# Performance work log

Measured on AMD Instinct MI355X. Metric: run time of the kernel, lower is better.

The kernel has to match this reference:

```python
import jax, jax.numpy as jnp
import numpy as np
from jax import lax

D_MODEL, D_INNER, D_STATE, D_CONV, DT_RANK = 1024, 2048, 16, 4, 64
B, L = 1, 2048


def setup_inputs() -> dict:
    key = jax.random.key(0)
    ks = jax.random.split(key, 10)
    s = lambda d: 1.0 / np.sqrt(d)
    return {
        "x": jax.random.normal(ks[0], (B, L, D_MODEL), jnp.float32),
        "W_in": jax.random.normal(ks[1], (D_MODEL, 2 * D_INNER), jnp.float32) * s(D_MODEL),
        "conv_w": jax.random.normal(ks[2], (D_INNER, D_CONV), jnp.float32) * s(D_CONV),
        "conv_b": jax.random.normal(ks[3], (D_INNER,), jnp.float32) * 0.01,
        "W_x": jax.random.normal(ks[4], (D_INNER, DT_RANK + 2 * D_STATE), jnp.float32) * s(D_INNER),
        "W_dt": jax.random.normal(ks[5], (DT_RANK, D_INNER), jnp.float32) * s(DT_RANK),
        "b_dt": jax.random.normal(ks[6], (D_INNER,), jnp.float32) * 0.01,
        # A = arange(1, d_state+1) repeated over d_inner; A_log = log(A)
        "A_log": jnp.log(jnp.tile(jnp.arange(1.0, D_STATE + 1.0, dtype=jnp.float32), (D_INNER, 1))),
        "D": jnp.ones((D_INNER,), jnp.float32),
        "W_out": jax.random.normal(ks[7], (D_INNER, D_MODEL), jnp.float32) * s(D_INNER),
    }


def reference(x, W_in, conv_w, conv_b, W_x, W_dt, b_dt, A_log, D, W_out):
    b, l, dm = x.shape
    di, n = A_log.shape[0], A_log.shape[1]
    # input projection + split into conv branch and gate residual
    x_and_res = x @ W_in                          # (b, l, 2*di)
    xc, res = x_and_res[..., :di], x_and_res[..., di:]
    # causal depthwise conv1d (left pad k-1, matches torch padding=k-1 + slice[:l])
    k = conv_w.shape[1]
    xp = jnp.pad(xc, ((0, 0), (k - 1, 0), (0, 0)))
    xconv = conv_b
    for j in range(k):
        xconv = xconv + xp[:, j:j + l, :] * conv_w[:, j]
    xs = jax.nn.silu(xconv)                       # (b, l, di)
    # selection parameters
    x_dbl = xs @ W_x                              # (b, l, dt_rank + 2n)
    dt_r = x_dbl[..., :DT_RANK]
    Bm = x_dbl[..., DT_RANK:DT_RANK + n]          # (b, l, n)
    Cm = x_dbl[..., DT_RANK + n:]                 # (b, l, n)
    dt = jax.nn.softplus(dt_r @ W_dt + b_dt)      # (b, l, di)
    A = -jnp.exp(A_log)                           # (di, n)
    # discretize
    dA = jnp.exp(jnp.einsum('bld,dn->bldn', dt, A))
    dBx = jnp.einsum('bld,bln->bldn', dt, Bm) * xs[..., None]
    # sequential state scan over time
    def step(h, inp):
        dA_t, dBx_t, C_t = inp                    # (b,di,n),(b,di,n),(b,n)
        h = dA_t * h + dBx_t
        y = jnp.einsum('bdn,bn->bd', h, C_t)
        return h, y
    h0 = jnp.zeros((b, di, n), x.dtype)
    hT, ys = lax.scan(step, h0, (dA.transpose(1, 0, 2, 3),
                                 dBx.transpose(1, 0, 2, 3),
                                 Cm.transpose(1, 0, 2)))
    y = ys.transpose(1, 0, 2) + xs * D            # (b, l, di)
    y = y * jax.nn.silu(res)
    out = y @ W_out                               # (b, l, d_model)
    return out, hT
```

## Files before the change

### kernel.cpp

```cpp
#include <hip/hip_runtime.h>
#include <math.h>

#define DM 1024
#define DI 2048
#define NS 16
#define DTR 64
#define LL 2048
#define NXDBL 96
#define NCHUNK 64
#define CHLEN 32
#define KSPLIT 8
#define G2KC 256

typedef unsigned short u16;
typedef __attribute__((ext_vector_type(8))) short short8;
typedef __attribute__((ext_vector_type(4))) float f32x4;

__device__ __forceinline__ float sigmoidf_(float x) { return 1.f / (1.f + __expf(-x)); }
__device__ __forceinline__ float siluf_(float x) { return x * sigmoidf_(x); }
__device__ __forceinline__ float softplus_fast(float x) {
    return fmaxf(x, 0.f) + __logf(1.f + __expf(-fabsf(x)));
}
__device__ __forceinline__ u16 f2b(float f) {
    unsigned u = __float_as_uint(f);
    return (u16)((u + 0x7FFFu + ((u >> 16) & 1u)) >> 16);
}

__global__ __launch_bounds__(256) void convert_plain(const float* __restrict__ src,
                                                     u16* __restrict__ dst) {
    const int i = (blockIdx.x * 256 + threadIdx.x) * 4;
    float4 v = *(const float4*)&src[i];
    u16 o[4] = {f2b(v.x), f2b(v.y), f2b(v.z), f2b(v.w)};
    *(ushort4*)&dst[i] = *(ushort4*)o;
}

__global__ __launch_bounds__(256) void convert_T(const float* __restrict__ src,
                                                 u16* __restrict__ dst, int R, int C) {
    __shared__ float t[32][33];
    const int tx = threadIdx.x & 31, ty = threadIdx.x >> 5;
    const int c0 = blockIdx.x * 32, r0 = blockIdx.y * 32;
#pragma unroll
    for (int i = 0; i < 4; i++)
        t[ty + i * 8][tx] = src[(size_t)(r0 + ty + i * 8) * C + c0 + tx];
    __syncthreads();
#pragma unroll
    for (int i = 0; i < 4; i++)
        dst[(size_t)(c0 + ty + i * 8) * R + r0 + tx] = f2b(t[tx][ty + i * 8]);
}

#define WAITV(N) asm volatile("s_waitcnt vmcnt(" #N ")" ::: "memory")
template <int EPI, int NSTEPS>
__global__ __launch_bounds__(256) void gemm_mfma(const u16* __restrict__ A,
                                                 const u16* __restrict__ Bt,
                                                 float* __restrict__ C0,
                                                 float* __restrict__ C1,
                                                 int M, int N, int lda) {
    __shared__ u16 As[3][128 * 32];
    __shared__ u16 Bs[3][128 * 32];
    const int tid = threadIdx.x;
    const int lane = tid & 63;
    const int wave = tid >> 6;
    const int bm = blockIdx.y * 128, bn = blockIdx.x * 128;
    const int wr = wave >> 1, wc = wave & 1;
    const int k_off = blockIdx.z * (NSTEPS * 32);

    f32x4 acc[4][4];
#pragma unroll
    for (int m = 0; m < 4; m++)
#pragma unroll
        for (int n = 0; n < 4; n++) acc[m][n] = (f32x4)0.f;

    const int srow = tid >> 2, skel = (tid & 3) << 3;
    const u16* Ag0 = A + (size_t)(bm + srow) * lda + k_off + skel;
    const u16* Ag1 = A + (size_t)(bm + 64 + srow) * lda + k_off + skel;
    const u16* Bg0 = Bt + (size_t)(bn + srow) * lda + k_off + skel;
    const u16* Bg1 = Bt + (size_t)(bn + 64 + srow) * lda + k_off + skel;
    u16* Asl = &As[0][0] + tid * 8;
    u16* Bsl = &Bs[0][0] + tid * 8;

    const int arow = (wr * 64 + (lane & 15)) * 32 + (lane >> 4) * 8;
    const int brow = (wc * 64 + (lane & 15)) * 32 + (lane >> 4) * 8;

#define STAGE(buf, ks)                                                               \
    do {                                                                             \
        __builtin_amdgcn_global_load_lds(                                            \
            (const __attribute__((address_space(1))) unsigned*)(Ag0 + (ks)),         \
            (__attribute__((address_space(3))) unsigned*)(Asl + (buf) * 4096),       \
            16, 0, 0);                                                               \
        __builtin_amdgcn_global_load_lds(                                            \
            (const __attribute__((address_space(1))) unsigned*)(Ag1 + (ks)),         \
            (__attribute__((address_space(3))) unsigned*)(Asl + (buf) * 4096 + 2048),\
            16, 0, 0);                                                               \
        __builtin_amdgcn_global_load_lds(                                            \
            (const __attribute__((address_space(1))) unsigned*)(Bg0 + (ks)),         \
            (__attribute__((address_space(3))) unsigned*)(Bsl + (buf) * 4096),       \
            16, 0, 0);                                                               \
        __builtin_amdgcn_global_load_lds(                                            \
            (const __attribute__((address_space(1))) unsigned*)(Bg1 + (ks)),         \
            (__attribute__((address_space(3))) unsigned*)(Bsl + (buf) * 4096 + 2048),\
            16, 0, 0);                                                               \
    } while (0)

#define COMPUTE(buf)                                                                 \
    do {                                                                             \
        short8 av[4], bv[4];                                                         \
        _Pragma("unroll") for (int m = 0; m < 4; m++)                                \
            av[m] = *(const short8*)&As[buf][arow + m * 512];                        \
        _Pragma("unroll") for (int n = 0; n < 4; n++)                                \
            bv[n] = *(const short8*)&Bs[buf][brow + n * 512];                        \
        _Pragma("unroll") for (int m = 0; m < 4; m++)                                \
            _Pragma("unroll") for (int n = 0; n < 4; n++)                            \
                acc[m][n] = __builtin_amdgcn_mfma_f32_16x16x32_bf16(av[m], bv[n],    \
                                                                    acc[m][n], 0, 0, 0); \
    } while (0)

    STAGE(0, 0);
    if (NSTEPS > 1) STAGE(1, 32);
#pragma unroll
    for (int s = 0; s < NSTEPS; ++s) {
        if (s + 2 < NSTEPS) {
            STAGE((s + 2) % 3, (s + 2) * 32);
            WAITV(8);
        } else if (s + 1 < NSTEPS) {
            WAITV(4);
        } else {
            WAITV(0);
        }
        __builtin_amdgcn_s_barrier();
        COMPUTE(s % 3);
        __builtin_amdgcn_s_barrier();
    }
#undef STAGE
#undef COMPUTE

    const int crow0 = bm + wr * 64 + (lane >> 4) * 4;
    const int ccol0 = bn + wc * 64 + (lane & 15);
    float* C0z = C0 + (size_t)blockIdx.z * M * N;
#pragma unroll
    for (int m = 0; m < 4; m++)
#pragma unroll
        for (int n = 0; n < 4; n++) {
            const int col = ccol0 + n * 16;
#pragma unroll
            for (int r = 0; r < 4; r++) {
                const int row = crow0 + m * 16 + r;
                const float v = acc[m][n][r];
                if (EPI == 1) {
                    if (col < DI)
                        C0[(size_t)row * DI + col] = v;
                    else
                        C1[(size_t)row * DI + col - DI] = v;
                } else {
                    C0z[(size_t)row * N + col] = v;
                }
            }
        }
}

__global__ __launch_bounds__(256) void gemm128_dt(const float* __restrict__ A,
                                                  const float* __restrict__ B,
                                                  const float* __restrict__ bias,
                                                  float* __restrict__ C,
                                                  int N, int K, int lda) {
    __shared__ float As[16][128];
    __shared__ float Bs[16][128];
    const int tid = threadIdx.x;
    const int bm = blockIdx.y * 128, bn = blockIdx.x * 128;
    const int ty = tid >> 4, tx = tid & 15;
    float acc[8][8];
#pragma unroll
    for (int i = 0; i < 8; i++)
#pragma unroll
        for (int j = 0; j < 8; j++) acc[i][j] = 0.f;

    const int ar = tid >> 2, ak = (tid & 3) << 2;
    const int bk = tid >> 5, bc = (tid & 31) << 2;

    for (int k0 = 0; k0 < K; k0 += 16) {
        float4 a0 = *(const float4*)&A[(size_t)(bm + ar) * lda + k0 + ak];
        float4 a1 = *(const float4*)&A[(size_t)(bm + ar + 64) * lda + k0 + ak];
        float4 b0 = *(const float4*)&B[(size_t)(k0 + bk) * N + bn + bc];
        float4 b1 = *(const float4*)&B[(size_t)(k0 + bk + 8) * N + bn + bc];
        __syncthreads();
        As[ak + 0][ar] = a0.x; As[ak + 1][ar] = a0.y;
        As[ak + 2][ar] = a0.z; As[ak + 3][ar] = a0.w;
        As[ak + 0][ar + 64] = a1.x; As[ak + 1][ar + 64] = a1.y;
        As[ak + 2][ar + 64] = a1.z; As[ak + 3][ar + 64] = a1.w;
        *(float4*)&Bs[bk][bc] = b0;
        *(float4*)&Bs[bk + 8][bc] = b1;
        __syncthreads();
#pragma unroll
        for (int k = 0; k < 16; k++) {
            float a[8], b[8];
            *(float4*)&a[0] = *(const float4*)&As[k][ty * 8];
            *(float4*)&a[4] = *(const float4*)&As[k][ty * 8 + 4];
            *(float4*)&b[0] = *(const float4*)&Bs[k][tx * 8];
            *(float4*)&b[4] = *(const float4*)&Bs[k][tx * 8 + 4];
#pragma unroll
            for (int i = 0; i < 8; i++)
#pragma unroll
                for (int j = 0; j < 8; j++) acc[i][j] = fmaf(a[i], b[j], acc[i][j]);
        }
    }
#pragma unroll
    for (int i = 0; i < 8; i++) {
        const int row = bm + ty * 8 + i;
#pragma unroll
        for (int j = 0; j < 8; j += 4) {
            const int col = bn + tx * 8 + j;
            const float4 bi = *(const float4*)&bias[col];
            float4 v = make_float4(softplus_fast(acc[i][j] + bi.x),
                                   softplus_fast(acc[i][j + 1] + bi.y),
                                   softplus_fast(acc[i][j + 2] + bi.z),
                                   softplus_fast(acc[i][j + 3] + bi.w));
            *(float4*)&C[(size_t)row * N + col] = v;
        }
    }
}

__global__ __launch_bounds__(256) void sum2(const float* __restrict__ p,
                                            float* __restrict__ out, int n) {
    const int i = (blockIdx.x * 256 + threadIdx.x) * 4;
    float4 a = *(const float4*)&p[i];
    float4 b = *(const float4*)&p[(size_t)n + i];
    float4 o = make_float4(a.x + b.x, a.y + b.y, a.z + b.z, a.w + b.w);
    *(float4*)&out[i] = o;
}

__global__ __launch_bounds__(256) void conv_silu(const float* __restrict__ xc,
                                                 const float* __restrict__ cw,
                                                 const float* __restrict__ cb,
                                                 float* __restrict__ xs) {
    const int gid = blockIdx.x * 256 + threadIdx.x;
    const int l = gid >> 11;
    const int d = gid & (DI - 1);
    const float4 w = *(const float4*)&cw[d * 4];
    float acc = cb[d];
    const float wj[4] = {w.x, w.y, w.z, w.w};
#pragma unroll
    for (int j = 0; j < 4; j++) {
        const int li = l + j - 3;
        if (li >= 0) acc = fmaf(xc[(size_t)li * DI + d], wj[j], acc);
    }
    xs[gid] = siluf_(acc);
}

__global__ __launch_bounds__(256) void gemm2_splitk(const float* __restrict__ xs,
                                                    const float* __restrict__ Wx,
                                                    float* __restrict__ part) {
    __shared__ float As[32][64];
    __shared__ float Bs[32 * 96];
    const int tid = threadIdx.x;
    const int bm = blockIdx.x * 64;
    const int ks = blockIdx.y;
    const int ty = tid >> 4, tx = tid & 15;
    float acc[4][6];
#pragma unroll
    for (int i = 0; i < 4; i++)
#pragma unroll
        for (int j = 0; j < 6; j++) acc[i][j] = 0.f;

    for (int kt = 0; kt < G2KC; kt += 32) {
        const int kbase = ks * G2KC + kt;
        float4 av[2];
        int arr[2], akk[2];
#pragma unroll
        for (int i = 0; i < 2; i++) {
            const int f = tid + 256 * i;
            arr[i] = f >> 3;
            akk[i] = (f & 7) << 2;
            av[i] = *(const float4*)&xs[(size_t)(bm + arr[i]) * DI + kbase + akk[i]];
        }
        float4 bv[3];
        int bro[3], bco[3];
#pragma unroll
        for (int i = 0; i < 3; i++) {
            const int f = tid + 256 * i;
            bro[i] = (f << 2) / 96;
            bco[i] = (f << 2) % 96;
            bv[i] = *(const float4*)&Wx[(size_t)(kbase + bro[i]) * 96 + bco[i]];
        }
        __syncthreads();
#pragma unroll
        for (int i = 0; i < 2; i++) {
            As[akk[i] + 0][arr[i]] = av[i].x;
            As[akk[i] + 1][arr[i]] = av[i].y;
            As[akk[i] + 2][arr[i]] = av[i].z;
            As[akk[i] + 3][arr[i]] = av[i].w;
        }
#pragma unroll
        for (int i = 0; i < 3; i++)
            *(float4*)&Bs[bro[i] * 96 + bco[i]] = bv[i];
        __syncthreads();
#pragma unroll
        for (int k = 0; k < 32; k++) {
            float a[4], b[6];
            *(float4*)&a[0] = *(const float4*)&As[k][ty * 4];
            *(float2*)&b[0] = *(const float2*)&Bs[k * 96 + tx * 6];
            *(float2*)&b[2] = *(const float2*)&Bs[k * 96 + tx * 6 + 2];
            *(float2*)&b[4] = *(const float2*)&Bs[k * 96 + tx * 6 + 4];
#pragma unroll
            for (int i = 0; i < 4; i++)
#pragma unroll
                for (int j = 0; j < 6; j++) acc[i][j] = fmaf(a[i], b[j], acc[i][j]);
        }
    }
#pragma unroll
    for (int i = 0; i < 4; i++) {
        const int row = bm + ty * 4 + i;
#pragma unroll
        for (int j = 0; j < 6; j++) {
            part[((size_t)ks * LL + row) * NXDBL + tx * 6 + j] = acc[i][j];
        }
    }
}

__global__ __launch_bounds__(256) void gemm2_reduce(const float* __restrict__ part,
                                                    float* __restrict__ xdbl) {
    const int gid = blockIdx.x * 256 + threadIdx.x;
    if (gid < LL * NXDBL) {
        float s = 0.f;
#pragma unroll
        for (int ks = 0; ks < KSPLIT; ks++) s += part[(size_t)ks * LL * NXDBL + gid];
        xdbl[gid] = s;
    }
}

__global__ __launch_bounds__(256) void scan_phase1(const float* __restrict__ dt,
                                                   const float* __restrict__ xs,
                                                   const float* __restrict__ xdbl,
                                                   const float* __restrict__ A_log,
                                                   float* __restrict__ chA,
                                                   float* __restrict__ chB) {
    const int g = blockIdx.x * 256 + threadIdx.x;
    const int d = g & (DI - 1);
    const int c = g >> 11;
    float An2[NS], ap[NS], bc[NS];
    {
        float al[NS];
#pragma unroll
        for (int q = 0; q < 4; q++)
            *(float4*)&al[q * 4] = *(const float4*)&A_log[d * NS + q * 4];
#pragma unroll
        for (int n = 0; n < NS; n++) {
            An2[n] = -__expf(al[n]) * 1.44269504f;
            ap[n] = 1.f;
            bc[n] = 0.f;
        }
    }
    const int l0 = c * CHLEN;
    for (int l = l0; l < l0 + CHLEN; ++l) {
        const float dtv = dt[(size_t)l * DI + d];
        const float xsv = xs[(size_t)l * DI + d];
        const float dx = dtv * xsv;
        float bv[NS];
#pragma unroll
        for (int q = 0; q < 4; q++)
            *(float4*)&bv[q * 4] = *(const float4*)&xdbl[(size_t)l * NXDBL + DTR + q * 4];
#pragma unroll
        for (int n = 0; n < NS; n++) {
            const float al = __builtin_amdgcn_exp2f(dtv * An2[n]);
            ap[n] *= al;
            bc[n] = fmaf(al, bc[n], dx * bv[n]);
        }
    }
    const size_t o = ((size_t)c * DI + d) * NS;
#pragma unroll
    for (int q = 0; q < 4; q++) {
        *(float4*)&chA[o + q * 4] = *(float4*)&ap[q * 4];
        *(float4*)&chB[o + q * 4] = *(float4*)&bc[q * 4];
    }
}

__global__ __launch_bounds__(256) void scan_phase2(float* __restrict__ chA,
                                                   const float* __restrict__ chB,
                                                   float* __restrict__ hT_out) {
    const int t = blockIdx.x * 256 + threadIdx.x;
    float h = 0.f;
#pragma unroll 4
    for (int c = 0; c < NCHUNK; ++c) {
        const size_t o = (size_t)c * DI * NS + t;
        const float a = chA[o];
        const float b = chB[o];
        chA[o] = h;
        h = fmaf(a, h, b);
    }
    hT_out[t] = h;
}

__global__ __launch_bounds__(256) void scan_phase3(const float* __restrict__ dt,
                                                   const float* __restrict__ xs,
                                                   const float* __restrict__ xdbl,
                                                   const float* __restrict__ A_log,
                                                   const float* __restrict__ h0,
                                                   const float* __restrict__ Dw,
                                                   const float* __restrict__ res,
                                                   u16* __restrict__ yb) {
    const int g = blockIdx.x * 256 + threadIdx.x;
    const int d = g & (DI - 1);
    const int c = g >> 11;
    float An2[NS], h[NS];
    {
        float al[NS];
#pragma unroll
        for (int q = 0; q < 4; q++)
            *(float4*)&al[q * 4] = *(const float4*)&A_log[d * NS + q * 4];
#pragma unroll
        for (int n = 0; n < NS; n++) An2[n] = -__expf(al[n]) * 1.44269504f;
    }
    const size_t ho = ((size_t)c * DI + d) * NS;
#pragma unroll
    for (int q = 0; q < 4; q++) *(float4*)&h[q * 4] = *(const float4*)&h0[ho + q * 4];
    const float Dd = Dw[d];
    const int l0 = c * CHLEN;
    for (int l = l0; l < l0 + CHLEN; ++l) {
        const float dtv = dt[(size_t)l * DI + d];
        const float xsv = xs[(size_t)l * DI + d];
        const float resv = res[(size_t)l * DI + d];
        const float dx = dtv * xsv;
        float bv[NS], cv[NS];
#pragma unroll
        for (int q = 0; q < 4; q++) {
            *(float4*)&bv[q * 4] = *(const float4*)&xdbl[(size_t)l * NXDBL + DTR + q * 4];
            *(float4*)&cv[q * 4] =
                *(const float4*)&xdbl[(size_t)l * NXDBL + DTR + NS + q * 4];
        }
#pragma unroll
        for (int n = 0; n < NS; n++) {
            const float al = __builtin_amdgcn_exp2f(dtv * An2[n]);
            h[n] = fmaf(al, h[n], dx * bv[n]);
        }
        float y0 = 0.f, y1 = 0.f, y2 = 0.f, y3 = 0.f;
#pragma unroll
        for (int n = 0; n < NS; n += 4) {
            y0 = fmaf(h[n + 0], cv[n + 0], y0);
            y1 = fmaf(h[n + 1], cv[n + 1], y1);
            y2 = fmaf(h[n + 2], cv[n + 2], y2);
            y3 = fmaf(h[n + 3], cv[n + 3], y3);
        }
        float yv = ((y0 + y1) + (y2 + y3)) + xsv * Dd;
        yv *= siluf_(resv);
        yb[(size_t)l * DI + d] = f2b(yv);
    }
}

extern "C" void kernel_launch(void* const* d_in, const int* in_sizes, int n_in,
                              void* d_out, int out_size, void* d_ws, size_t ws_size,
                              hipStream_t stream) {
    const float* x = (const float*)d_in[0];
    const float* W_in = (const float*)d_in[1];
    const float* conv_w = (const float*)d_in[2];
    const float* conv_b = (const float*)d_in[3];
    const float* W_x = (const float*)d_in[4];
    const float* W_dt = (const float*)d_in[5];
    const float* b_dt = (const float*)d_in[6];
    const float* A_log = (const float*)d_in[7];
    const float* Dw = (const float*)d_in[8];
    const float* W_out = (const float*)d_in[9];
    float* out = (float*)d_out;

    float* ws = (float*)d_ws;
    float* xc = ws;
    float* res = ws + 4194304;
    float* xs = ws + 8388608;
    float* dt = ws + 12582912;
    float* xdbl = ws + 16777216;
    float* chA = ws + 16973824;
    float* chB = ws + 19070976;
    u16* xb = (u16*)chB;
    float* part = chB;
    u16* W_outT_b = (u16*)chB;
    u16* W_inT_b = (u16*)dt;
    u16* yb = (u16*)xc;
    float* g4part = res;

    convert_plain<<<(LL * DM) / 1024, 256, 0, stream>>>(x, xb);
    convert_T<<<dim3(2 * DI / 32, DM / 32), 256, 0, stream>>>(W_in, W_inT_b, DM, 2 * DI);
    gemm_mfma<1, DM / 32><<<dim3(2 * DI / 128, LL / 128), 256, 0, stream>>>(
        xb, W_inT_b, xc, res, LL, 2 * DI, DM);
    conv_silu<<<(LL * DI) / 256, 256, 0, stream>>>(xc, conv_w, conv_b, xs);
    gemm2_splitk<<<dim3(LL / 64, KSPLIT), 256, 0, stream>>>(xs, W_x, part);
    gemm2_reduce<<<(LL * NXDBL + 255) / 256, 256, 0, stream>>>(part, xdbl);
    gemm128_dt<<<dim3(DI / 128, LL / 128), 256, 0, stream>>>(xdbl, W_dt, b_dt, dt,
                                                             DI, DTR, NXDBL);
    scan_phase1<<<(DI * NCHUNK) / 256, 256, 0, stream>>>(dt, xs, xdbl, A_log, chA, chB);
    scan_phase2<<<(DI * NS) / 256, 256, 0, stream>>>(chA, chB, out + (size_t)LL * DM);
    convert_T<<<dim3(DM / 32, DI / 32), 256, 0, stream>>>(W_out, W_outT_b, DI, DM);
    scan_phase3<<<(DI * NCHUNK) / 256, 256, 0, stream>>>(dt, xs, xdbl, A_log, chA, Dw,
                                                         res, yb);
    gemm_mfma<0, DI / 64><<<dim3(DM / 128, LL / 128, 2), 256, 0, stream>>>(
        yb, W_outT_b, g4part, nullptr, LL, DM, DI);
    sum2<<<(LL * DM) / 1024, 256, 0, stream>>>(g4part, out, LL * DM);
}
```

Before: 201.7 us.

## Move x_dbl projection to bf16 MFMA split-K GEMM and swizzle LDS layout

Replaces the fp32 FMA split-K GEMM for xs@W_x with the existing bf16 MFMA GEMM kernel. To feed it, conv_silu now also emits a bf16 copy of xs, W_x is transposed and zero-padded to 128 columns, and a 16-way split-K runs with a matching reduce. It also XOR-swizzles the LDS layout in the MFMA GEMM to reduce bank conflicts on fragment reads, which affects all three GEMMs. Workspace buffers are given distinct regions instead of aliasing. In exchange it adds extra launches and lowers the precision of the selection parameters to bf16.

```diff
diff --git a/kernel.cpp b/kernel.cpp
--- a/kernel.cpp
+++ b/kernel.cpp
@@ -9,8 +9,6 @@
 #define NXDBL 96
 #define NCHUNK 64
 #define CHLEN 32
-#define KSPLIT 8
-#define G2KC 256
 
 typedef unsigned short u16;
 typedef __attribute__((ext_vector_type(8))) short short8;
@@ -46,6 +44,11 @@
 #pragma unroll
     for (int i = 0; i < 4; i++)
         dst[(size_t)(c0 + ty + i * 8) * R + r0 + tx] = f2b(t[tx][ty + i * 8]);
+}
+
+__global__ __launch_bounds__(256) void fill_zero_u16(u16* __restrict__ p, int n) {
+    const int i = blockIdx.x * 256 + threadIdx.x;
+    if (i < n) p[i] = 0;
 }
 
 #define WAITV(N) asm volatile("s_waitcnt vmcnt(" #N ")" ::: "memory")
@@ -70,7 +73,9 @@
 #pragma unroll
         for (int n = 0; n < 4; n++) acc[m][n] = (f32x4)0.f;
 
-    const int srow = tid >> 2, skel = (tid & 3) << 3;
+    const int srow = tid >> 2;
+    const int swz = (tid >> 3) & 3;
+    const int skel = (((tid & 3) ^ swz) << 3);
     const u16* Ag0 = A + (size_t)(bm + srow) * lda + k_off + skel;
     const u16* Ag1 = A + (size_t)(bm + 64 + srow) * lda + k_off + skel;
     const u16* Bg0 = Bt + (size_t)(bn + srow) * lda + k_off + skel;
@@ -78,8 +83,9 @@
     u16* Asl = &As[0][0] + tid * 8;
     u16* Bsl = &Bs[0][0] + tid * 8;
 
-    const int arow = (wr * 64 + (lane & 15)) * 32 + (lane >> 4) * 8;
-    const int brow = (wc * 64 + (lane & 15)) * 32 + (lane >> 4) * 8;
+    const int rsw = (lane >> 1) & 3;
+    const int arow = (wr * 64 + (lane & 15)) * 32 + (((lane >> 4) ^ rsw) << 3);
+    const int brow = (wc * 64 + (lane & 15)) * 32 + (((lane >> 4) ^ rsw) << 3);
 
 #define STAGE(buf, ks)                                                               \
     do {                                                                             \
@@ -223,14 +229,27 @@
     const int i = (blockIdx.x * 256 + threadIdx.x) * 4;
     float4 a = *(const float4*)&p[i];
     float4 b = *(const float4*)&p[(size_t)n + i];
-    float4 o = make_float4(a.x + b.x, a.y + b.y, a.z + b.z, a.w + b.w);
-    *(float4*)&out[i] = o;
+    *(float4*)&out[i] = make_float4(a.x + b.x, a.y + b.y, a.z + b.z, a.w + b.w);
+}
+
+__global__ __launch_bounds__(256) void g2reduce(const float* __restrict__ part,
+                                                float* __restrict__ xdbl) {
+    const int gid = blockIdx.x * 256 + threadIdx.x;
+    if (gid < LL * NXDBL) {
+        const int row = gid / NXDBL;
+        const int col = gid - row * NXDBL;
+        float s = 0.f;
+#pragma unroll
+        for (int z = 0; z < 16; z++) s += part[((size_t)z * LL + row) * 128 + col];
+        xdbl[gid] = s;
+    }
 }
 
 __global__ __launch_bounds__(256) void conv_silu(const float* __restrict__ xc,
                                                  const float* __restrict__ cw,
                                                  const float* __restrict__ cb,
-                                                 float* __restrict__ xs) {
+                                                 float* __restrict__ xs,
+                                                 u16* __restrict__ xsb) {
     const int gid = blockIdx.x * 256 + threadIdx.x;
     const int l = gid >> 11;
     const int d = gid & (DI - 1);
@@ -242,88 +261,9 @@
         const int li = l + j - 3;
         if (li >= 0) acc = fmaf(xc[(size_t)li * DI + d], wj[j], acc);
     }
-    xs[gid] = siluf_(acc);
-}
-
-__global__ __launch_bounds__(256) void gemm2_splitk(const float* __restrict__ xs,
-                                                    const float* __restrict__ Wx,
-                                                    float* __restrict__ part) {
-    __shared__ float As[32][64];
-    __shared__ float Bs[32 * 96];
-    const int tid = threadIdx.x;
-    const int bm = blockIdx.x * 64;
-    const int ks = blockIdx.y;
-    const int ty = tid >> 4, tx = tid & 15;
-    float acc[4][6];
-#pragma unroll
-    for (int i = 0; i < 4; i++)
-#pragma unroll
-        for (int j = 0; j < 6; j++) acc[i][j] = 0.f;
-
-    for (int kt = 0; kt < G2KC; kt += 32) {
-        const int kbase = ks * G2KC + kt;
-        float4 av[2];
-        int arr[2], akk[2];
-#pragma unroll
-        for (int i = 0; i < 2; i++) {
-            const int f = tid + 256 * i;
-            arr[i] = f >> 3;
-            akk[i] = (f & 7) << 2;
-            av[i] = *(const float4*)&xs[(size_t)(bm + arr[i]) * DI + kbase + akk[i]];
-        }
-        float4 bv[3];
-        int bro[3], bco[3];
-#pragma unroll
-        for (int i = 0; i < 3; i++) {
-            const int f = tid + 256 * i;
-            bro[i] = (f << 2) / 96;
-            bco[i] = (f << 2) % 96;
-            bv[i] = *(const float4*)&Wx[(size_t)(kbase + bro[i]) * 96 + bco[i]];
-        }
-        __syncthreads();
-#pragma unroll
-        for (int i = 0; i < 2; i++) {
-            As[akk[i] + 0][arr[i]] = av[i].x;
-            As[akk[i] + 1][arr[i]] = av[i].y;
-            As[akk[i] + 2][arr[i]] = av[i].z;
-            As[akk[i] + 3][arr[i]] = av[i].w;
-        }
-#pragma unroll
-        for (int i = 0; i < 3; i++)
-            *(float4*)&Bs[bro[i] * 96 + bco[i]] = bv[i];
-        __syncthreads();
-#pragma unroll
-        for (int k = 0; k < 32; k++) {
-            float a[4], b[6];
-            *(float4*)&a[0] = *(const float4*)&As[k][ty * 4];
-            *(float2*)&b[0] = *(const float2*)&Bs[k * 96 + tx * 6];
-            *(float2*)&b[2] = *(const float2*)&Bs[k * 96 + tx * 6 + 2];
-            *(float2*)&b[4] = *(const float2*)&Bs[k * 96 + tx * 6 + 4];
-#pragma unroll
-            for (int i = 0; i < 4; i++)
-#pragma unroll
-                for (int j = 0; j < 6; j++) acc[i][j] = fmaf(a[i], b[j], acc[i][j]);
-        }
-    }
-#pragma unroll
-    for (int i = 0; i < 4; i++) {
-        const int row = bm + ty * 4 + i;
-#pragma unroll
-        for (int j = 0; j < 6; j++) {
-            part[((size_t)ks * LL + row) * NXDBL + tx * 6 + j] = acc[i][j];
-        }
-    }
-}
-
-__global__ __launch_bounds__(256) void gemm2_reduce(const float* __restrict__ part,
-                                                    float* __restrict__ xdbl) {
-    const int gid = blockIdx.x * 256 + threadIdx.x;
-    if (gid < LL * NXDBL) {
-        float s = 0.f;
-#pragma unroll
-        for (int ks = 0; ks < KSPLIT; ks++) s += part[(size_t)ks * LL * NXDBL + gid];
-        xdbl[gid] = s;
-    }
+    const float s = siluf_(acc);
+    xs[gid] = s;
+    xsb[gid] = f2b(s);
 }
 
 __global__ __launch_bounds__(256) void scan_phase1(const float* __restrict__ dt,
@@ -460,27 +400,32 @@
     float* out = (float*)d_out;
 
     float* ws = (float*)d_ws;
-    float* xc = ws;
-    float* res = ws + 4194304;
-    float* xs = ws + 8388608;
-    float* dt = ws + 12582912;
-    float* xdbl = ws + 16777216;
-    float* chA = ws + 16973824;
-    float* chB = ws + 19070976;
-    u16* xb = (u16*)chB;
-    float* part = chB;
-    u16* W_outT_b = (u16*)chB;
-    u16* W_inT_b = (u16*)dt;
-    u16* yb = (u16*)xc;
-    float* g4part = res;
+    float* xc       = ws;
+    float* res      = ws + 4194304;
+    float* xs       = ws + 8388608;
+    float* dt       = ws + 12582912;
+    float* xdbl     = ws + 16777216;
+    float* chA      = ws + 16973824;
+    float* chB      = ws + 19070976;
+    u16*   xb       = (u16*)(ws + 21168128);
+    u16*   W_inT_b  = (u16*)(ws + 22216704);
+    u16*   W_outT_b = (u16*)(ws + 24313856);
+    u16*   xs_b     = (u16*)(ws + 25362432);
+    u16*   W_xT_pad = (u16*)(ws + 27459584);
+    float* g2part   = ws + 27590656;
+    float* g4part   = ws + 31784960;
+    u16*   yb       = (u16*)(ws + 35979264);
 
     convert_plain<<<(LL * DM) / 1024, 256, 0, stream>>>(x, xb);
     convert_T<<<dim3(2 * DI / 32, DM / 32), 256, 0, stream>>>(W_in, W_inT_b, DM, 2 * DI);
     gemm_mfma<1, DM / 32><<<dim3(2 * DI / 128, LL / 128), 256, 0, stream>>>(
         xb, W_inT_b, xc, res, LL, 2 * DI, DM);
-    conv_silu<<<(LL * DI) / 256, 256, 0, stream>>>(xc, conv_w, conv_b, xs);
-    gemm2_splitk<<<dim3(LL / 64, KSPLIT), 256, 0, stream>>>(xs, W_x, part);
-    gemm2_reduce<<<(LL * NXDBL + 255) / 256, 256, 0, stream>>>(part, xdbl);
+    conv_silu<<<(LL * DI) / 256, 256, 0, stream>>>(xc, conv_w, conv_b, xs, xs_b);
+    fill_zero_u16<<<(32 * DI + 255) / 256, 256, 0, stream>>>(W_xT_pad + 96 * DI, 32 * DI);
+    convert_T<<<dim3(NXDBL / 32, DI / 32), 256, 0, stream>>>(W_x, W_xT_pad, DI, NXDBL);
+    gemm_mfma<0, 4><<<dim3(1, LL / 128, 16), 256, 0, stream>>>(
+        xs_b, W_xT_pad, g2part, nullptr, LL, 128, DI);
+    g2reduce<<<(LL * NXDBL + 255) / 256, 256, 0, stream>>>(g2part, xdbl);
     gemm128_dt<<<dim3(DI / 128, LL / 128), 256, 0, stream>>>(xdbl, W_dt, b_dt, dt,
                                                              DI, DTR, NXDBL);
     scan_phase1<<<(DI * NCHUNK) / 256, 256, 0, stream>>>(dt, xs, xdbl, A_log, chA, chB);
```

Result: faster. 179.8 us (-10.9%).
